# Kernel optimization log

Hardware: AMD Instinct MI355X
Metric: run time of the kernel (lower is better)

## Reference

```python
import jax, jax.numpy as jnp
import numpy as np

EMBED_DIM = 1024
NUM_HEADS = 16
HEAD_DIM = EMBED_DIM // NUM_HEADS


def setup_inputs() -> dict:
    key = jax.random.key(0)
    ks = jax.random.split(key, 7)
    B, S, E = 2, 2048, EMBED_DIM
    scale = 1.0 / np.sqrt(E)
    x = jax.random.normal(ks[0], (B, S, E), dtype=jnp.float32)
    Wq = jax.random.normal(ks[1], (E, E), dtype=jnp.float32) * scale
    Wk = jax.random.normal(ks[2], (E, E), dtype=jnp.float32) * scale
    Wv = jax.random.normal(ks[3], (E, E), dtype=jnp.float32) * scale
    bq = jax.random.normal(ks[4], (E,), dtype=jnp.float32) * 0.01
    bk = jax.random.normal(ks[5], (E,), dtype=jnp.float32) * 0.01
    bv = jax.random.normal(ks[6], (E,), dtype=jnp.float32) * 0.01
    return {"x": x, "Wq": Wq, "bq": bq, "Wk": Wk, "bk": bk, "Wv": Wv, "bv": bv}


def reference(x, Wq, bq, Wk, bk, Wv, bv):
    B, S, E = x.shape
    H, D = NUM_HEADS, HEAD_DIM
    # QKV projections (nn.Linear: x @ W^T + b; W sampled square so we use x @ W + b equivalently as the learned map)
    q = (x @ Wq + bq).reshape(B, S, H, D)
    k = (x @ Wk + bk).reshape(B, S, H, D)
    v = (x @ Wv + bv).reshape(B, S, H, D)
    # scores: [B, H, S, S] -- NOTE: original applies no 1/sqrt(d) scaling
    scores = jnp.einsum("bqhd,bkhd->bhqk", q, k)
    attn = jax.nn.softmax(scores, axis=-1)
    out = jnp.einsum("bhqk,bkhd->bqhd", attn, v)
    return out.reshape(B, S, E)
```

## Files before the change

kernel.cpp:

```cpp
#include <hip/hip_runtime.h>

#define E_DIM 1024
#define NHEADS 16
#define HDIM 64
#define BATCH 2
#define SEQ 2048
#define M_TOT (BATCH*SEQ)

typedef _Float16 f16;
typedef _Float16 half4 __attribute__((ext_vector_type(4)));
typedef _Float16 half8 __attribute__((ext_vector_type(8)));
typedef _Float16 half2v __attribute__((ext_vector_type(2)));
typedef float floatx4 __attribute__((ext_vector_type(4)));

#define MFMA16x32(a,b,c) __builtin_amdgcn_mfma_f32_16x16x32_f16((a),(b),(c),0,0,0)

__device__ __forceinline__ void gll16(const f16* gsrc, f16* ldst) {
    __builtin_amdgcn_global_load_lds(
        (const __attribute__((address_space(1))) void*)gsrc,
        (__attribute__((address_space(3))) void*)ldst, 16, 0, 0);
}

__global__ __launch_bounds__(256) void cvt_x(const float* __restrict__ x,
                                             f16* __restrict__ xh) {
    size_t i = ((size_t)blockIdx.x * 256 + threadIdx.x) * 8;
    float4 a = *(const float4*)&x[i];
    float4 b = *(const float4*)&x[i + 4];
    half8 h = {(f16)a.x,(f16)a.y,(f16)a.z,(f16)a.w,
               (f16)b.x,(f16)b.y,(f16)b.z,(f16)b.w};
    *(half8*)&xh[i] = h;
}

__global__ __launch_bounds__(256) void transpose_w(
    const float* __restrict__ Wq, const float* __restrict__ Wk,
    const float* __restrict__ Wv,
    f16* __restrict__ WTq, f16* __restrict__ WTk, f16* __restrict__ WTv)
{
    const int z = blockIdx.z;
    const float* W = (z == 0) ? Wq : (z == 1) ? Wk : Wv;
    f16* WT        = (z == 0) ? WTq : (z == 1) ? WTk : WTv;

    const int k0 = blockIdx.x * 64, n0 = blockIdx.y * 64;
    const int tid = threadIdx.x;
    __shared__ f16 T[64][68];

    {
        const int tr = tid >> 4, tc = tid & 15;
        float4 f4[4];
        #pragma unroll
        for (int i = 0; i < 4; i++)
            f4[i] = *(const float4*)&W[(size_t)(k0 + tr * 4 + i) * E_DIM + n0 + tc * 4];
        #pragma unroll
        for (int j = 0; j < 4; j++) {
            float e0 = (j==0)?f4[0].x:(j==1)?f4[0].y:(j==2)?f4[0].z:f4[0].w;
            float e1 = (j==0)?f4[1].x:(j==1)?f4[1].y:(j==2)?f4[1].z:f4[1].w;
            float e2 = (j==0)?f4[2].x:(j==1)?f4[2].y:(j==2)?f4[2].z:f4[2].w;
            float e3 = (j==0)?f4[3].x:(j==1)?f4[3].y:(j==2)?f4[3].z:f4[3].w;
            half4 h = {(f16)e0, (f16)e1, (f16)e2, (f16)e3};
            *(half4*)&T[tc * 4 + j][tr * 4] = h;
        }
    }
    __syncthreads();
    {
        const int nn = tid >> 2, kk = (tid & 3) * 16;
        half8 a = *(const half8*)&T[nn][kk];
        half8 b = *(const half8*)&T[nn][kk + 8];
        f16* dst = &WT[(size_t)(n0 + nn) * E_DIM + k0 + kk];
        *(half8*)dst = a;
        *(half8*)(dst + 8) = b;
    }
}

__global__ __launch_bounds__(256) void qkv_gemm(
    const f16* __restrict__ xh, const f16* __restrict__ WTall,
    const float* __restrict__ bq, const float* __restrict__ bk,
    const float* __restrict__ bv,
    f16* __restrict__ qh, f16* __restrict__ kh, f16* __restrict__ vh)
{
    const int flat = blockIdx.x;
    const int rb = (flat & 7) * 96 + (flat >> 3);
    const int z   = rb >> 8;
    const int ntl = rb & 7;
    const int mt  = (rb >> 3) & 31;

    const float* bias = (z == 0) ? bq : (z == 1) ? bk : bv;
    f16* out          = (z == 0) ? qh : (z == 1) ? kh : vh;

    const int m0 = mt * 128;
    const int n0g = z * 1024 + ntl * 128;
    const int tid = threadIdx.x;
    const int lane = tid & 63;
    const int w  = tid >> 6;
    const int wm = w >> 1, wn = w & 1;
    const int g  = lane >> 4, r = lane & 15;

    __shared__ f16 Al[128 * 64];
    __shared__ f16 Bl[128 * 64];

    const int lrow = lane >> 3;
    const int lcol = ((lane & 7) ^ lrow) * 8;
    const f16* asrc = xh    + (size_t)(m0  + lrow) * E_DIM + lcol;
    const f16* bsrc = WTall + (size_t)(n0g + lrow) * E_DIM + lcol;

    floatx4 acc[4][4];
    #pragma unroll
    for (int i = 0; i < 4; i++)
        #pragma unroll
        for (int j = 0; j < 4; j++)
            acc[i][j] = (floatx4){0.f, 0.f, 0.f, 0.f};

    for (int k0 = 0; k0 < E_DIM; k0 += 64) {
        if (k0) __syncthreads();
        #pragma unroll
        for (int t = 0; t < 4; t++) {
            int c = w * 4 + t;
            gll16(asrc + (size_t)c * 8 * E_DIM + k0, Al + c * 512);
            gll16(bsrc + (size_t)c * 8 * E_DIM + k0, Bl + c * 512);
        }
        __syncthreads();

        #pragma unroll
        for (int ks = 0; ks < 64; ks += 32) {
            half8 af[4], bf[4];
            #pragma unroll
            for (int i = 0; i < 4; i++) {
                int row = wm * 64 + i * 16 + r;
                af[i] = *(const half8*)&Al[row * 64 + ((ks + g * 8) ^ ((row & 7) << 3))];
            }
            #pragma unroll
            for (int j = 0; j < 4; j++) {
                int row = wn * 64 + j * 16 + r;
                bf[j] = *(const half8*)&Bl[row * 64 + ((ks + g * 8) ^ ((row & 7) << 3))];
            }
            #pragma unroll
            for (int i = 0; i < 4; i++)
                #pragma unroll
                for (int j = 0; j < 4; j++)
                    acc[i][j] = MFMA16x32(af[i], bf[j], acc[i][j]);
        }
    }

    #pragma unroll
    for (int j = 0; j < 4; j++) {
        int col = ntl * 128 + wn * 64 + j * 16 + r;
        float bb = bias[col];
        #pragma unroll
        for (int i = 0; i < 4; i++)
            #pragma unroll
            for (int rr = 0; rr < 4; rr++) {
                int row = m0 + wm * 64 + i * 16 + g * 4 + rr;
                out[(size_t)row * E_DIM + col] = (f16)(acc[i][j][rr] + bb);
            }
    }
}

__global__ __launch_bounds__(256) void qkv_proj_v2(
    const float* __restrict__ x,
    const f16* __restrict__ WTq, const f16* __restrict__ WTk,
    const f16* __restrict__ WTv,
    const float* __restrict__ bq, const float* __restrict__ bk,
    const float* __restrict__ bv,
    f16* __restrict__ qh, f16* __restrict__ kh, f16* __restrict__ vh)
{
    const int flat = blockIdx.x;
    const int rb = (flat & 7) * 96 + (flat >> 3);
    const int nt = rb & 7;
    const int mt = (rb >> 3) & 31;
    const int z  = rb >> 8;

    const f16* WT     = (z == 0) ? WTq : (z == 1) ? WTk : WTv;
    const float* bias = (z == 0) ? bq : (z == 1) ? bk : bv;
    f16* out          = (z == 0) ? qh : (z == 1) ? kh : vh;

    const int m0 = mt * 128, n0 = nt * 128;
    const int tid = threadIdx.x;
    const int lane = tid & 63;
    const int w  = tid >> 6;
    const int wm = w >> 1, wn = w & 1;
    const int g  = lane >> 4, r = lane & 15;

    __shared__ f16 Al[128 * 32];
    __shared__ f16 Bl[128 * 32];

    floatx4 acc[4][4];
    #pragma unroll
    for (int i = 0; i < 4; i++)
        #pragma unroll
        for (int j = 0; j < 4; j++)
            acc[i][j] = (floatx4){0.f, 0.f, 0.f, 0.f};

    for (int k0 = 0; k0 < E_DIM; k0 += 32) {
        #pragma unroll
        for (int it = 0; it < 2; it++) {
            int idx = tid + it * 256;
            int mm = idx >> 2, kc = (idx & 3) * 8;
            const float* s = &x[(size_t)(m0 + mm) * E_DIM + k0 + kc];
            float4 u = *(const float4*)s;
            float4 v = *(const float4*)(s + 4);
            half8 hv = {(f16)u.x,(f16)u.y,(f16)u.z,(f16)u.w,
                        (f16)v.x,(f16)v.y,(f16)v.z,(f16)v.w};
            *(half8*)&Al[mm * 32 + (kc ^ (((mm >> 2) & 3) << 3))] = hv;
        }
        #pragma unroll
        for (int it = 0; it < 2; it++) {
            int idx = tid + it * 256;
            int nn = idx >> 2, kc = (idx & 3) * 8;
            half8 hv = *(const half8*)&WT[(size_t)(n0 + nn) * E_DIM + k0 + kc];
            *(half8*)&Bl[nn * 32 + (kc ^ (((nn >> 2) & 3) << 3))] = hv;
        }
        __syncthreads();

        half8 af[4], bf[4];
        #pragma unroll
        for (int i = 0; i < 4; i++) {
            int row = wm * 64 + i * 16 + r;
            af[i] = *(const half8*)&Al[row * 32 + ((g * 8) ^ (((row >> 2) & 3) << 3))];
        }
        #pragma unroll
        for (int j = 0; j < 4; j++) {
            int row = wn * 64 + j * 16 + r;
            bf[j] = *(const half8*)&Bl[row * 32 + ((g * 8) ^ (((row >> 2) & 3) << 3))];
        }
        #pragma unroll
        for (int i = 0; i < 4; i++)
            #pragma unroll
            for (int j = 0; j < 4; j++)
                acc[i][j] = MFMA16x32(af[i], bf[j], acc[i][j]);
        __syncthreads();
    }

    #pragma unroll
    for (int j = 0; j < 4; j++) {
        int col = n0 + wn * 64 + j * 16 + r;
        float bb = bias[col];
        #pragma unroll
        for (int i = 0; i < 4; i++)
            #pragma unroll
            for (int rr = 0; rr < 4; rr++) {
                int row = m0 + wm * 64 + i * 16 + g * 4 + rr;
                out[(size_t)row * E_DIM + col] = (f16)(acc[i][j][rr] + bb);
            }
    }
}

__global__ __launch_bounds__(512, 2) void attn(
    const f16* __restrict__ qh, const f16* __restrict__ kh,
    const f16* __restrict__ vh, float* __restrict__ out)
{
    const int flat = blockIdx.x;
    const int rb = (flat & 7) * 32 + (flat >> 3);
    const int qt = rb & 7;
    const int hh = (rb >> 3) & 15;
    const int b  = rb >> 7;
    const int q0 = qt * 256;

    const int tid = threadIdx.x;
    const int lane = tid & 63;
    const int w = tid >> 6;
    const int g = lane >> 4, r = lane & 15;

    __shared__ f16 K_s[64 * 64];
    __shared__ f16 V_s[64 * 64];

    const size_t base = ((size_t)b * SEQ) * E_DIM + (size_t)hh * HDIM;

    half8 aq[2][2];
    #pragma unroll
    for (int qf = 0; qf < 2; qf++) {
        const f16* qp = &qh[base + (size_t)(q0 + w * 32 + qf * 16 + r) * E_DIM];
        aq[qf][0] = *(const half8*)&qp[g * 8];
        aq[qf][1] = *(const half8*)&qp[32 + g * 8];
    }

    const int krow = w * 8 + (lane >> 3);
    const int kcol = ((lane & 7) ^ (lane >> 3)) * 8;
    const f16* kg0 = kh + base + (size_t)krow * E_DIM + kcol;
    f16* klds = K_s + w * 512;

    const int vp = tid >> 4, vdc = (tid & 15) * 4;
    const int kv0 = vp * 2;
    const int kvp0 = (kv0 & 3) | (((kv0 >> 4) & 1) << 2) |
                     (((kv0 >> 2) & 3) << 3) | ((kv0 >> 5) << 5);
    const f16* vg0 = vh + base + (size_t)kv0 * E_DIM + vdc;

    float m_run[2] = {-1e30f, -1e30f}, l_run[2] = {0.f, 0.f};
    floatx4 acco[2][4];
    #pragma unroll
    for (int qf = 0; qf < 2; qf++)
        #pragma unroll
        for (int dj = 0; dj < 4; dj++)
            acco[qf][dj] = (floatx4){0.f, 0.f, 0.f, 0.f};

    for (int kt = 0; kt < SEQ; kt += 64) {
        if (kt) __syncthreads();
        gll16(kg0 + (size_t)kt * E_DIM, klds);
        {
            const f16* vsrc = vg0 + (size_t)kt * E_DIM;
            half4 v0 = *(const half4*)vsrc;
            half4 v1 = *(const half4*)(vsrc + E_DIM);
            #pragma unroll
            for (int e = 0; e < 4; e++) {
                int d = vdc + e;
                int swv = ((d ^ (d >> 3)) & 7) << 3;
                half2v pr = {v0[e], v1[e]};
                *(half2v*)&V_s[d * 64 + (kvp0 ^ swv)] = pr;
            }
        }
        __syncthreads();

        floatx4 sct[2][4];
        #pragma unroll
        for (int qf = 0; qf < 2; qf++)
            #pragma unroll
            for (int kb = 0; kb < 4; kb++)
                sct[qf][kb] = (floatx4){0.f, 0.f, 0.f, 0.f};
        #pragma unroll
        for (int kb = 0; kb < 4; kb++) {
            int kr2 = kb * 16 + r;
            int swk = (kr2 & 7) << 3;
            const f16* kb_ = &K_s[kr2 * 64];
            half8 kf0 = *(const half8*)&kb_[(g * 8) ^ swk];
            half8 kf1 = *(const half8*)&kb_[(32 + g * 8) ^ swk];
            #pragma unroll
            for (int qf = 0; qf < 2; qf++) {
                sct[qf][kb] = MFMA16x32(kf0, aq[qf][0], sct[qf][kb]);
                sct[qf][kb] = MFMA16x32(kf1, aq[qf][1], sct[qf][kb]);
            }
        }

        half8 pa[2][2];
        #pragma unroll
        for (int qf = 0; qf < 2; qf++) {
            float pm = sct[qf][0][0];
            #pragma unroll
            for (int kb = 0; kb < 4; kb++)
                #pragma unroll
                for (int rr = 0; rr < 4; rr++)
                    pm = fmaxf(pm, sct[qf][kb][rr]);
            pm = fmaxf(pm, __shfl_xor(pm, 16, 64));
            pm = fmaxf(pm, __shfl_xor(pm, 32, 64));
            float mn = fmaxf(m_run[qf], pm);
            float alpha = __expf(m_run[qf] - mn);
            m_run[qf] = mn;
            float rs = 0.f;
            #pragma unroll
            for (int kb = 0; kb < 4; kb++)
                #pragma unroll
                for (int rr = 0; rr < 4; rr++) {
                    float e = __expf(sct[qf][kb][rr] - mn);
                    sct[qf][kb][rr] = e;
                    rs += e;
                }
            rs += __shfl_xor(rs, 16, 64);
            rs += __shfl_xor(rs, 32, 64);
            l_run[qf] = l_run[qf] * alpha + rs;
            #pragma unroll
            for (int dj = 0; dj < 4; dj++)
                #pragma unroll
                for (int rr = 0; rr < 4; rr++)
                    acco[qf][dj][rr] *= alpha;
            #pragma unroll
            for (int h = 0; h < 2; h++) {
                half8 t = {(f16)sct[qf][h*2][0],   (f16)sct[qf][h*2][1],
                           (f16)sct[qf][h*2][2],   (f16)sct[qf][h*2][3],
                           (f16)sct[qf][h*2+1][0], (f16)sct[qf][h*2+1][1],
                           (f16)sct[qf][h*2+1][2], (f16)sct[qf][h*2+1][3]};
                pa[qf][h] = t;
            }
        }

        #pragma unroll
        for (int dj = 0; dj < 4; dj++) {
            int d = dj * 16 + r;
            int swv = ((d ^ (d >> 3)) & 7) << 3;
            const f16* vb_ = &V_s[d * 64];
            half8 vf0 = *(const half8*)&vb_[(g * 8) ^ swv];
            half8 vf1 = *(const half8*)&vb_[(32 + g * 8) ^ swv];
            #pragma unroll
            for (int qf = 0; qf < 2; qf++) {
                acco[qf][dj] = MFMA16x32(vf0, pa[qf][0], acco[qf][dj]);
                acco[qf][dj] = MFMA16x32(vf1, pa[qf][1], acco[qf][dj]);
            }
        }
    }

    #pragma unroll
    for (int qf = 0; qf < 2; qf++) {
        float inv = 1.f / l_run[qf];
        int row = q0 + w * 32 + qf * 16 + r;
        float* orow = out + (size_t)(b * SEQ + row) * E_DIM + hh * HDIM;
        #pragma unroll
        for (int dj = 0; dj < 4; dj++) {
            float4 st = {acco[qf][dj][0] * inv, acco[qf][dj][1] * inv,
                         acco[qf][dj][2] * inv, acco[qf][dj][3] * inv};
            *(float4*)&orow[dj * 16 + g * 4] = st;
        }
    }
}

extern "C" void kernel_launch(void* const* d_in, const int* in_sizes, int n_in,
                              void* d_out, int out_size, void* d_ws, size_t ws_size,
                              hipStream_t stream) {
    const float* x  = (const float*)d_in[0];
    const float* Wq = (const float*)d_in[1];
    const float* bq = (const float*)d_in[2];
    const float* Wk = (const float*)d_in[3];
    const float* bk = (const float*)d_in[4];
    const float* Wv = (const float*)d_in[5];
    const float* bv = (const float*)d_in[6];
    float* out = (float*)d_out;

    const size_t qkv_elems = (size_t)M_TOT * E_DIM;
    const size_t w_elems   = (size_t)E_DIM * E_DIM;
    f16* qh  = (f16*)d_ws;
    f16* kh  = qh + qkv_elems;
    f16* vh  = kh + qkv_elems;
    f16* WTq = vh + qkv_elems;
    f16* WTk = WTq + w_elems;
    f16* WTv = WTk + w_elems;
    f16* xh  = WTv + w_elems;
    const size_t need_v3  = (3 * qkv_elems + 3 * w_elems + qkv_elems) * sizeof(f16);
    const size_t need_v2  = (3 * qkv_elems + 3 * w_elems) * sizeof(f16);
    if (ws_size < need_v2) return;

    if (ws_size >= need_v3) {
        cvt_x<<<dim3(M_TOT * E_DIM / (256 * 8)), 256, 0, stream>>>(x, xh);
        transpose_w<<<dim3(16, 16, 3), 256, 0, stream>>>(Wq, Wk, Wv, WTq, WTk, WTv);
        qkv_gemm<<<dim3((E_DIM / 128) * (M_TOT / 128) * 3), 256, 0, stream>>>(
            xh, WTq, bq, bk, bv, qh, kh, vh);
    } else {
        transpose_w<<<dim3(16, 16, 3), 256, 0, stream>>>(Wq, Wk, Wv, WTq, WTk, WTv);
        qkv_proj_v2<<<dim3((E_DIM / 128) * (M_TOT / 128) * 3), 256, 0, stream>>>(
            x, WTq, WTk, WTv, bq, bk, bv, qh, kh, vh);
    }
    attn<<<dim3((SEQ / 256) * NHEADS * BATCH), 512, 0, stream>>>(qh, kh, vh, out);
}
```

Baseline: 183.2 us.

## Double-buffer K/V tiles in attention, halve query tile, add lazy rescale

The attention kernel now double-buffers K and V in shared memory, prefetching the next tile while the current one is computed, which cuts one barrier per iteration. Each wave now handles 16 query rows instead of 32, so the grid doubles to 512 blocks and launch bounds allow 4 blocks per CU. The online softmax skips rescaling the accumulators unless the running max grows by more than 8, and MFMA sections are raised in priority with s_setprio. In exchange, each K/V tile is reused by half as many query rows, so K/V traffic per query doubles, and the lazy rescale lets exponents drift up to e^8 before they are cast to fp16.

```diff
diff --git a/kernel.cpp b/kernel.cpp
--- a/kernel.cpp
+++ b/kernel.cpp
@@ -243,39 +243,37 @@
     }
 }
 
-__global__ __launch_bounds__(512, 2) void attn(
+__global__ __launch_bounds__(512, 4) void attn(
     const f16* __restrict__ qh, const f16* __restrict__ kh,
     const f16* __restrict__ vh, float* __restrict__ out)
 {
     const int flat = blockIdx.x;
-    const int rb = (flat & 7) * 32 + (flat >> 3);
-    const int qt = rb & 7;
-    const int hh = (rb >> 3) & 15;
-    const int b  = rb >> 7;
-    const int q0 = qt * 256;
+    const int rb = (flat & 7) * 64 + (flat >> 3);
+    const int qt = rb & 15;
+    const int hh = (rb >> 4) & 15;
+    const int b  = rb >> 8;
+    const int q0 = qt * 128;
 
     const int tid = threadIdx.x;
     const int lane = tid & 63;
     const int w = tid >> 6;
     const int g = lane >> 4, r = lane & 15;
 
-    __shared__ f16 K_s[64 * 64];
-    __shared__ f16 V_s[64 * 64];
+    __shared__ f16 K_s[2][64 * 64];
+    __shared__ f16 V_s[2][64 * 64];
 
     const size_t base = ((size_t)b * SEQ) * E_DIM + (size_t)hh * HDIM;
 
-    half8 aq[2][2];
-    #pragma unroll
-    for (int qf = 0; qf < 2; qf++) {
-        const f16* qp = &qh[base + (size_t)(q0 + w * 32 + qf * 16 + r) * E_DIM];
-        aq[qf][0] = *(const half8*)&qp[g * 8];
-        aq[qf][1] = *(const half8*)&qp[32 + g * 8];
-    }
-
-    const int krow = w * 8 + (lane >> 3);
-    const int kcol = ((lane & 7) ^ (lane >> 3)) * 8;
-    const f16* kg0 = kh + base + (size_t)krow * E_DIM + kcol;
-    f16* klds = K_s + w * 512;
+    half8 aq[2];
+    {
+        const f16* qp = &qh[base + (size_t)(q0 + w * 16 + r) * E_DIM];
+        aq[0] = *(const half8*)&qp[g * 8];
+        aq[1] = *(const half8*)&qp[32 + g * 8];
+    }
+
+    const int klrow = lane >> 3;
+    const int kcol = ((lane & 7) ^ klrow) * 8;
+    const f16* kg0 = kh + base + (size_t)(w * 8 + klrow) * E_DIM + kcol;
 
     const int vp = tid >> 4, vdc = (tid & 15) * 4;
     const int kv0 = vp * 2;
@@ -283,116 +281,130 @@
                      (((kv0 >> 2) & 3) << 3) | ((kv0 >> 5) << 5);
     const f16* vg0 = vh + base + (size_t)kv0 * E_DIM + vdc;
 
-    float m_run[2] = {-1e30f, -1e30f}, l_run[2] = {0.f, 0.f};
-    floatx4 acco[2][4];
+    float m_run = -1e30f, l_run = 0.f;
+    floatx4 acco[4];
     #pragma unroll
-    for (int qf = 0; qf < 2; qf++)
-        #pragma unroll
-        for (int dj = 0; dj < 4; dj++)
-            acco[qf][dj] = (floatx4){0.f, 0.f, 0.f, 0.f};
-
-    for (int kt = 0; kt < SEQ; kt += 64) {
-        if (kt) __syncthreads();
-        gll16(kg0 + (size_t)kt * E_DIM, klds);
-        {
-            const f16* vsrc = vg0 + (size_t)kt * E_DIM;
-            half4 v0 = *(const half4*)vsrc;
-            half4 v1 = *(const half4*)(vsrc + E_DIM);
+    for (int dj = 0; dj < 4; dj++) acco[dj] = (floatx4){0.f, 0.f, 0.f, 0.f};
+
+    const int NT = SEQ / 64;
+
+    gll16(kg0, &K_s[0][w * 512]);
+    {
+        half4 v0 = *(const half4*)vg0;
+        half4 v1 = *(const half4*)(vg0 + E_DIM);
+        #pragma unroll
+        for (int e = 0; e < 4; e++) {
+            int d = vdc + e;
+            int swv = ((d ^ (d >> 3)) & 7) << 3;
+            half2v pr = {v0[e], v1[e]};
+            *(half2v*)&V_s[0][d * 64 + (kvp0 ^ swv)] = pr;
+        }
+    }
+    __syncthreads();
+
+    for (int t = 0; t < NT; t++) {
+        const int cur = t & 1;
+        const bool pf = (t + 1 < NT);
+        half4 v0n, v1n;
+        if (pf) {
+            gll16(kg0 + (size_t)(t + 1) * 64 * E_DIM, &K_s[cur ^ 1][w * 512]);
+            const f16* vsrc = vg0 + (size_t)(t + 1) * 64 * E_DIM;
+            v0n = *(const half4*)vsrc;
+            v1n = *(const half4*)(vsrc + E_DIM);
+        }
+
+        floatx4 sct[4];
+        __builtin_amdgcn_s_setprio(1);
+        #pragma unroll
+        for (int kb = 0; kb < 4; kb++) {
+            int kr2 = kb * 16 + r;
+            int swk = (kr2 & 7) << 3;
+            const f16* kb_ = &K_s[cur][kr2 * 64];
+            half8 kf0 = *(const half8*)&kb_[(g * 8) ^ swk];
+            half8 kf1 = *(const half8*)&kb_[(32 + g * 8) ^ swk];
+            floatx4 c = (floatx4){0.f, 0.f, 0.f, 0.f};
+            c = MFMA16x32(kf0, aq[0], c);
+            c = MFMA16x32(kf1, aq[1], c);
+            sct[kb] = c;
+        }
+        __builtin_amdgcn_s_setprio(0);
+
+        float pm = sct[0][0];
+        #pragma unroll
+        for (int kb = 0; kb < 4; kb++)
+            #pragma unroll
+            for (int rr = 0; rr < 4; rr++)
+                pm = fmaxf(pm, sct[kb][rr]);
+        pm = fmaxf(pm, __shfl_xor(pm, 16, 64));
+        pm = fmaxf(pm, __shfl_xor(pm, 32, 64));
+        if (!__all(pm - m_run <= 8.f)) {
+            float mn = fmaxf(m_run, pm);
+            float alpha = __expf(m_run - mn);
+            m_run = mn;
+            l_run *= alpha;
+            #pragma unroll
+            for (int dj = 0; dj < 4; dj++)
+                #pragma unroll
+                for (int rr = 0; rr < 4; rr++)
+                    acco[dj][rr] *= alpha;
+        }
+        float rs = 0.f;
+        #pragma unroll
+        for (int kb = 0; kb < 4; kb++)
+            #pragma unroll
+            for (int rr = 0; rr < 4; rr++) {
+                float e = __expf(sct[kb][rr] - m_run);
+                sct[kb][rr] = e;
+                rs += e;
+            }
+        rs += __shfl_xor(rs, 16, 64);
+        rs += __shfl_xor(rs, 32, 64);
+        l_run += rs;
+
+        half8 pa[2];
+        #pragma unroll
+        for (int h = 0; h < 2; h++) {
+            half8 tv = {(f16)sct[h*2][0],   (f16)sct[h*2][1],
+                        (f16)sct[h*2][2],   (f16)sct[h*2][3],
+                        (f16)sct[h*2+1][0], (f16)sct[h*2+1][1],
+                        (f16)sct[h*2+1][2], (f16)sct[h*2+1][3]};
+            pa[h] = tv;
+        }
+
+        if (pf) {
             #pragma unroll
             for (int e = 0; e < 4; e++) {
                 int d = vdc + e;
                 int swv = ((d ^ (d >> 3)) & 7) << 3;
-                half2v pr = {v0[e], v1[e]};
-                *(half2v*)&V_s[d * 64 + (kvp0 ^ swv)] = pr;
-            }
-        }
-        __syncthreads();
-
-        floatx4 sct[2][4];
-        #pragma unroll
-        for (int qf = 0; qf < 2; qf++)
-            #pragma unroll
-            for (int kb = 0; kb < 4; kb++)
-                sct[qf][kb] = (floatx4){0.f, 0.f, 0.f, 0.f};
-        #pragma unroll
-        for (int kb = 0; kb < 4; kb++) {
-            int kr2 = kb * 16 + r;
-            int swk = (kr2 & 7) << 3;
-            const f16* kb_ = &K_s[kr2 * 64];
-            half8 kf0 = *(const half8*)&kb_[(g * 8) ^ swk];
-            half8 kf1 = *(const half8*)&kb_[(32 + g * 8) ^ swk];
-            #pragma unroll
-            for (int qf = 0; qf < 2; qf++) {
-                sct[qf][kb] = MFMA16x32(kf0, aq[qf][0], sct[qf][kb]);
-                sct[qf][kb] = MFMA16x32(kf1, aq[qf][1], sct[qf][kb]);
-            }
-        }
-
-        half8 pa[2][2];
-        #pragma unroll
-        for (int qf = 0; qf < 2; qf++) {
-            float pm = sct[qf][0][0];
-            #pragma unroll
-            for (int kb = 0; kb < 4; kb++)
-                #pragma unroll
-                for (int rr = 0; rr < 4; rr++)
-                    pm = fmaxf(pm, sct[qf][kb][rr]);
-            pm = fmaxf(pm, __shfl_xor(pm, 16, 64));
-            pm = fmaxf(pm, __shfl_xor(pm, 32, 64));
-            float mn = fmaxf(m_run[qf], pm);
-            float alpha = __expf(m_run[qf] - mn);
-            m_run[qf] = mn;
-            float rs = 0.f;
-            #pragma unroll
-            for (int kb = 0; kb < 4; kb++)
-                #pragma unroll
-                for (int rr = 0; rr < 4; rr++) {
-                    float e = __expf(sct[qf][kb][rr] - mn);
-                    sct[qf][kb][rr] = e;
-                    rs += e;
-                }
-            rs += __shfl_xor(rs, 16, 64);
-            rs += __shfl_xor(rs, 32, 64);
-            l_run[qf] = l_run[qf] * alpha + rs;
-            #pragma unroll
-            for (int dj = 0; dj < 4; dj++)
-                #pragma unroll
-                for (int rr = 0; rr < 4; rr++)
-                    acco[qf][dj][rr] *= alpha;
-            #pragma unroll
-            for (int h = 0; h < 2; h++) {
-                half8 t = {(f16)sct[qf][h*2][0],   (f16)sct[qf][h*2][1],
-                           (f16)sct[qf][h*2][2],   (f16)sct[qf][h*2][3],
-                           (f16)sct[qf][h*2+1][0], (f16)sct[qf][h*2+1][1],
-                           (f16)sct[qf][h*2+1][2], (f16)sct[qf][h*2+1][3]};
-                pa[qf][h] = t;
-            }
-        }
-
+                half2v pr = {v0n[e], v1n[e]};
+                *(half2v*)&V_s[cur ^ 1][d * 64 + (kvp0 ^ swv)] = pr;
+            }
+        }
+
+        __builtin_amdgcn_s_setprio(1);
         #pragma unroll
         for (int dj = 0; dj < 4; dj++) {
             int d = dj * 16 + r;
             int swv = ((d ^ (d >> 3)) & 7) << 3;
-            const f16* vb_ = &V_s[d * 64];
+            const f16* vb_ = &V_s[cur][d * 64];
             half8 vf0 = *(const half8*)&vb_[(g * 8) ^ swv];
             half8 vf1 = *(const half8*)&vb_[(32 + g * 8) ^ swv];
-            #pragma unroll
-            for (int qf = 0; qf < 2; qf++) {
-                acco[qf][dj] = MFMA16x32(vf0, pa[qf][0], acco[qf][dj]);
-                acco[qf][dj] = MFMA16x32(vf1, pa[qf][1], acco[qf][dj]);
-            }
-        }
-    }
-
-    #pragma unroll
-    for (int qf = 0; qf < 2; qf++) {
-        float inv = 1.f / l_run[qf];
-        int row = q0 + w * 32 + qf * 16 + r;
+            acco[dj] = MFMA16x32(vf0, pa[0], acco[dj]);
+            acco[dj] = MFMA16x32(vf1, pa[1], acco[dj]);
+        }
+        __builtin_amdgcn_s_setprio(0);
+
+        __syncthreads();
+    }
+
+    {
+        float inv = 1.f / l_run;
+        int row = q0 + w * 16 + r;
         float* orow = out + (size_t)(b * SEQ + row) * E_DIM + hh * HDIM;
         #pragma unroll
         for (int dj = 0; dj < 4; dj++) {
-            float4 st = {acco[qf][dj][0] * inv, acco[qf][dj][1] * inv,
-                         acco[qf][dj][2] * inv, acco[qf][dj][3] * inv};
+            float4 st = {acco[dj][0] * inv, acco[dj][1] * inv,
+                         acco[dj][2] * inv, acco[dj][3] * inv};
             *(float4*)&orow[dj * 16 + g * 4] = st;
         }
     }
@@ -433,5 +445,5 @@
         qkv_proj_v2<<<dim3((E_DIM / 128) * (M_TOT / 128) * 3), 256, 0, stream>>>(
             x, WTq, WTk, WTv, bq, bk, bv, qh, kh, vh);
     }
-    attn<<<dim3((SEQ / 256) * NHEADS * BATCH), 512, 0, stream>>>(qh, kh, vh, out);
-}
+    attn<<<dim3((SEQ / 128) * NHEADS * BATCH), 512, 0, stream>>>(qh, kh, vh, out);
+}
```

Result: faster. 173.5 us (-5.3%).
